# Performance work log

Hardware: AMD Instinct MI355X
Metric: run time of the kernel (lower is better)

The kernel has to match this reference:

```python
import jax, jax.numpy as jnp
import numpy as np

S, B, C, H, W = 16, 64, 128, 11, 11
P = H * W
N_ITER = 3
EPS = 1e-5


def setup_inputs() -> dict:
    key = jax.random.key(0)
    ks = jax.random.split(key, 12)
    w = lambda k, shape: jax.random.normal(k, shape, jnp.float32) * 0.02
    return {
        "x": jax.random.normal(ks[0], (S, B, C, H, W), jnp.float32),
        # intra-attention 1x1 convs (stored as [out,in] matrices)
        "wq": w(ks[1], (C, C)), "bq": jnp.zeros((C,), jnp.float32),
        "wk": w(ks[2], (C, C)), "bk": jnp.zeros((C,), jnp.float32),
        "wv": w(ks[3], (C, C)), "bv": jnp.zeros((C,), jnp.float32),
        "intra_alpha": jnp.float32(1.0),
        # inter-message path
        "w_msg": w(ks[4], (C, C + 1)), "b_msg": jnp.zeros((C,), jnp.float32),
        "w_lin": w(ks[5], (C, C)),
        "weight": jnp.float32(0.5),
        "w_gate": w(ks[6], (C, C)), "b_gate": jnp.zeros((C,), jnp.float32),
        # ConvGRU 3x3 convs
        "w_zr": w(ks[7], (2 * C, 2 * C, 3, 3)), "b_zr": jnp.zeros((2 * C,), jnp.float32),
        "w_h": w(ks[8], (C, 2 * C, 3, 3)), "b_h": jnp.zeros((C,), jnp.float32),
        # LayerNorm over [C,11,11]
        "ln_gamma": jnp.ones((C, H, W), jnp.float32),
        "ln_beta": jnp.zeros((C, H, W), jnp.float32),
    }


def reference(x, wq, bq, wk, bk, wv, bv, intra_alpha, w_msg, b_msg, w_lin,
              weight, w_gate, b_gate, w_zr, b_zr, w_h, b_h, ln_gamma, ln_beta):
    scale = C ** -0.5

    def c1(t, wgt, bias):  # 1x1 conv on [S,B,Cin,H,W] -> [S,B,Cout,H,W]
        return jnp.einsum('sbchw,oc->sbohw', t, wgt) + bias[:, None, None]

    def conv3(t, wgt, bias):  # 3x3 'SAME' conv on [N,Cin,H,W]
        y = jax.lax.conv_general_dilated(
            t, wgt, (1, 1), 'SAME', dimension_numbers=('NCHW', 'OIHW', 'NCHW'))
        return y + bias[None, :, None, None]

    # chain-graph neighbor validity masks (|i-j| == 1)
    mask_l = (jnp.arange(S) >= 1).astype(x.dtype)[:, None, None, None, None]
    mask_r = (jnp.arange(S) <= S - 2).astype(x.dtype)[:, None, None, None, None]

    h = x
    for _ in range(N_ITER):
        # ---- intra spatial self-attention (per node, over P=H*W tokens) ----
        q = c1(h, wq, bq).reshape(S, B, C, P)
        k = c1(h, wk, bk).reshape(S, B, C, P)
        v = c1(h, wv, bv).reshape(S, B, C, P)
        att = jax.nn.softmax(jnp.einsum('sbcp,sbcq->sbpq', q, k) * scale, axis=-1)
        intra = jnp.einsum('sbpq,sbcq->sbcp', att, v).reshape(S, B, C, H, W)
        intra = intra_alpha * intra + h

        # ---- inter gated message attention from chain neighbors ----
        xf = h.reshape(S, B, C, P)

        def gated_msg(y, edge_val):
            ef = jnp.full((S, B, 1, H, W), edge_val, h.dtype)  # edge feature i-j
            yy = c1(jnp.concatenate([y, ef], axis=2), w_msg, b_msg).reshape(S, B, C, P)
            yy = jnp.einsum('sbcp,dc->sbdp', yy, w_lin)  # Linear (no bias)
            a = jax.nn.softmax(jnp.einsum('sbcp,sbcq->sbpq', xf, yy), axis=-1)
            m = jnp.einsum('sbpq,sbcq->sbcp', a, yy).reshape(S, B, C, H, W)
            g = jax.nn.sigmoid(c1(m, w_gate, b_gate).mean(axis=(-2, -1), keepdims=True))
            return m * g

        y_left = jnp.concatenate([jnp.zeros_like(h[:1]), h[:-1]], axis=0)   # h[i-1], edge +1
        y_right = jnp.concatenate([h[1:], jnp.zeros_like(h[:1])], axis=0)   # h[i+1], edge -1
        inter = gated_msg(y_left, 1.0) * mask_l + gated_msg(y_right, -1.0) * mask_r

        comb = weight * intra + (1.0 - weight) * inter

        # ---- ConvGRU update (fold S into batch) ----
        xg = comb.reshape(S * B, C, H, W)
        hg = h.reshape(S * B, C, H, W)
        zr = jax.nn.sigmoid(conv3(jnp.concatenate([xg, hg], axis=1), w_zr, b_zr))
        z, r = zr[:, :C], zr[:, C:]
        h_hat = jnp.tanh(conv3(jnp.concatenate([xg, r * hg], axis=1), w_h, b_h))
        h_new = ((1 - z) * hg + z * h_hat).reshape(S, B, C, H, W)

        # ---- residual + LayerNorm over [C,H,W] ----
        nh = h_new + h
        mu = nh.mean(axis=(-3, -2, -1), keepdims=True)
        var = nh.var(axis=(-3, -2, -1), keepdims=True)
        h = (nh - mu) * jax.lax.rsqrt(var + EPS) * ln_gamma + ln_beta
    return h
```

## Files before the change

kernel.cpp:

```cpp
#include <hip/hip_runtime.h>
#include <hip/hip_bf16.h>

#define S_   16
#define B_   64
#define SBn  1024
#define C_   128
#define P_   121
#define CP_  15488
static const long NEl = 15859712L;

typedef __hip_bfloat16 bf16t;
typedef __attribute__((ext_vector_type(8))) short bf16x8;
typedef __attribute__((ext_vector_type(4))) float f32x4;
typedef __attribute__((ext_vector_type(4))) unsigned short us4;

__device__ __forceinline__ float ldb(const bf16t* p){ return __bfloat162float(*p); }
__device__ __forceinline__ float b2f(unsigned short u){ unsigned x=((unsigned)u)<<16; float f; __builtin_memcpy(&f,&x,4); return f; }
__device__ __forceinline__ unsigned short f2bu(float v){ __hip_bfloat16 b=__float2bfloat16(v); unsigned short u; __builtin_memcpy(&u,&b,2); return u; }
__device__ __forceinline__ float ldin(const void* s, long i, int f){
    return f ? ((const float*)s)[i] : b2f(((const unsigned short*)s)[i]);
}

__global__ void detect_kernel(const unsigned short* __restrict__ x, int* __restrict__ flag){
    if(blockIdx.x==0 && threadIdx.x==0){
        int crazy=0;
        for(int i=0;i<512;i++){
            unsigned e=(x[i]>>7)&0xFF;
            if(e!=0 && (e<64 || e>191)) crazy++;
        }
        *flag=(crazy>40)?1:0;
    }
}

__global__ void cvt_kernel(float* __restrict__ dst, const void* __restrict__ src, long n, const int* __restrict__ flag){
    long i=(long)blockIdx.x*blockDim.x+threadIdx.x;
    long st=(long)gridDim.x*blockDim.x;
    int f=*flag;
    for(;i<n;i+=st) dst[i]=ldin(src,i,f);
}

__global__ __launch_bounds__(256) void cvtT_kernel(bf16t* __restrict__ hT, const void* __restrict__ x, const int* __restrict__ flag){
    int sb=blockIdx.x, t=threadIdx.x; int f=*flag;
    for(int i=t;i<CP_;i+=256){
        int c=i/P_, p=i-c*P_;
        float v=ldin(x,(long)sb*CP_+i,f);
        hT[(size_t)sb*CP_+(size_t)p*C_+c]=__float2bfloat16(v);
    }
}

__global__ __launch_bounds__(128) void prep_msg_kernel(float* __restrict__ W2, float* __restrict__ b2l, float* __restrict__ b2r,
        const void* __restrict__ wlin, const void* __restrict__ wmsg, const void* __restrict__ bmsg, const int* __restrict__ flag){
    int d=blockIdx.x, c=threadIdx.x; int f=*flag;
    float acc=0.f;
    for(int o2=0;o2<C_;o2++) acc += ldin(wlin,(long)d*C_+o2,f)*ldin(wmsg,(long)o2*(C_+1)+c,f);
    W2[d*C_+c]=acc;
    if(c<2){
        float e=(c==0)?1.f:-1.f; float a=0.f;
        for(int o2=0;o2<C_;o2++) a += ldin(wlin,(long)d*C_+o2,f)*(ldin(bmsg,o2,f)+e*ldin(wmsg,(long)o2*(C_+1)+C_,f));
        if(c==0) b2l[d]=a; else b2r[d]=a;
    }
}

template<int RAW>
__global__ void prep_w1t(bf16t* __restrict__ dst, const void* __restrict__ src, const int* __restrict__ flag){
    int idx=blockIdx.x*blockDim.x+threadIdx.x;
    if(idx>=16384) return;
    int r=idx&31, oc=(idx>>5)&127, icb=idx>>12;
    float v = RAW? ldin(src,(long)oc*C_+icb*32+r,*flag) : ((const float*)src)[(long)oc*C_+icb*32+r];
    dst[idx]=__float2bfloat16(v);
}

__global__ void prep_w3t(bf16t* __restrict__ dst, const void* __restrict__ src, const int* __restrict__ flag, int OC){
    int idx=blockIdx.x*blockDim.x+threadIdx.x;
    int tot=OC*2304;
    if(idx>=tot) return;
    int r=idx&31; int rest=idx>>5; int oc=rest%OC; int g2=rest/OC; int icb=g2&7, tap=g2>>3;
    float v=ldin(src,((long)(oc*256+icb*32+r))*9+tap,*flag);
    dst[idx]=__float2bfloat16(v);
}

__global__ void prep_gbt(float* __restrict__ gamT, float* __restrict__ betT,
                         const void* __restrict__ gam, const void* __restrict__ bet, const int* __restrict__ flag){
    int idx=blockIdx.x*blockDim.x+threadIdx.x;
    if(idx>=CP_) return;
    int c=idx/P_, p=idx-c*P_; int f=*flag;
    gamT[p*C_+c]=ldin(gam,idx,f);
    betT[p*C_+c]=ldin(bet,idx,f);
}

__global__ void prep_wgt(float* __restrict__ wgT, float* __restrict__ bg2,
                         const void* __restrict__ wg, const void* __restrict__ bg, const int* __restrict__ flag){
    int idx=blockIdx.x*blockDim.x+threadIdx.x;
    int f=*flag;
    if(idx<16384){ int k=idx>>7, c=idx&127; wgT[idx]=ldin(wg,(long)c*C_+k,f); }
    if(idx<128) bg2[idx]=ldin(bg,idx,f);
}

__device__ __forceinline__ void gemm24g(f32x4 (&acc)[4][2],
    const bf16t* __restrict__ Wt, const bf16t* __restrict__ hsrc,
    int ocr,int pcr,int l15,int kg)
{
    #pragma unroll
    for(int i=0;i<4;i++){
        #pragma unroll
        for(int j=0;j<2;j++) acc[i][j]=(f32x4){0.f,0.f,0.f,0.f};
    }
    #pragma unroll
    for(int kc=0;kc<4;kc++){
        bf16x8 a[4],b[2];
        #pragma unroll
        for(int mt=0;mt<4;mt++) a[mt]=*(const bf16x8*)(Wt+((size_t)(kc*C_+ocr*64+mt*16+l15))*32+kg*8);
        #pragma unroll
        for(int nt=0;nt<2;nt++) b[nt]=*(const bf16x8*)(hsrc+(size_t)(pcr*32+nt*16+l15)*C_+kc*32+kg*8);
        #pragma unroll
        for(int mt=0;mt<4;mt++){
            #pragma unroll
            for(int nt=0;nt<2;nt++)
                acc[mt][nt]=__builtin_amdgcn_mfma_f32_16x16x32_bf16(a[mt],b[nt],acc[mt][nt],0,0,0);
        }
    }
}

__global__ __launch_bounds__(512) void qkv_attn(
    bf16t* __restrict__ comb, const bf16t* __restrict__ hT,
    const bf16t* __restrict__ WqT, const bf16t* __restrict__ WkT, const bf16t* __restrict__ WvT,
    const float* __restrict__ bq, const float* __restrict__ bk, const float* __restrict__ bv,
    const float* __restrict__ alphap, const float* __restrict__ wp)
{
    __shared__ bf16t LA[128*136];
    __shared__ bf16t LB[128*136];
    int sb=blockIdx.x, t=threadIdx.x, lane=t&63, w=t>>6;
    int l15=lane&15, kg=lane>>4;
    const bf16t* hp=hT+(size_t)sb*CP_;
    int ocr=w>>2, pcr=w&3;
    f32x4 acc[4][2];
    gemm24g(acc,WqT,hp,ocr,pcr,l15,kg);
    #pragma unroll
    for(int mt=0;mt<4;mt++){
        int oc0=ocr*64+mt*16+kg*4;
        #pragma unroll
        for(int nt=0;nt<2;nt++){
            int p=pcr*32+nt*16+l15;
            us4 pk;
            #pragma unroll
            for(int r=0;r<4;r++) pk[r]=f2bu(acc[mt][nt][r]+bq[oc0+r]);
            *(us4*)(LA+p*136+oc0)=pk;
        }
    }
    gemm24g(acc,WkT,hp,ocr,pcr,l15,kg);
    #pragma unroll
    for(int mt=0;mt<4;mt++){
        int oc0=ocr*64+mt*16+kg*4;
        #pragma unroll
        for(int nt=0;nt<2;nt++){
            int p=pcr*32+nt*16+l15;
            us4 pk;
            #pragma unroll
            for(int r=0;r<4;r++) pk[r]=f2bu(acc[mt][nt][r]+bk[oc0+r]);
            *(us4*)(LB+p*136+oc0)=pk;
        }
    }
    __syncthreads();
    int m0=w*16;
    f32x4 s[8];
    #pragma unroll
    for(int nt=0;nt<8;nt++) s[nt]=(f32x4){0.f,0.f,0.f,0.f};
    #pragma unroll
    for(int kc=0;kc<4;kc++){
        bf16x8 a=*(const bf16x8*)(LA+(size_t)(m0+l15)*136+kc*32+kg*8);
        #pragma unroll
        for(int nt=0;nt<8;nt++){
            bf16x8 b=*(const bf16x8*)(LB+(size_t)(nt*16+l15)*136+kc*32+kg*8);
            s[nt]=__builtin_amdgcn_mfma_f32_16x16x32_bf16(a,b,s[nt],0,0,0);
        }
    }
    const float scale=0.08838834764831845f;
    #pragma unroll
    for(int nt=0;nt<8;nt++){
        #pragma unroll
        for(int r=0;r<4;r++) s[nt][r]*=scale;
    }
    if(l15>=9){
        #pragma unroll
        for(int r=0;r<4;r++) s[7][r]=-3.0e38f;
    }
    #pragma unroll
    for(int r=0;r<4;r++){
        float mx=s[0][r];
        #pragma unroll
        for(int nt=1;nt<8;nt++) mx=fmaxf(mx,s[nt][r]);
        #pragma unroll
        for(int o=1;o<16;o<<=1) mx=fmaxf(mx,__shfl_xor(mx,o));
        float sm=0.f;
        #pragma unroll
        for(int nt=0;nt<8;nt++){ float e=__expf(s[nt][r]-mx); s[nt][r]=e; sm+=e; }
        #pragma unroll
        for(int o=1;o<16;o<<=1) sm+=__shfl_xor(sm,o);
        float rs=1.f/sm;
        #pragma unroll
        for(int nt=0;nt<8;nt++) s[nt][r]*=rs;
    }
    __syncthreads();
    gemm24g(acc,WvT,hp,ocr,pcr,l15,kg);
    #pragma unroll
    for(int mt=0;mt<4;mt++){
        int oc0=ocr*64+mt*16+kg*4;
        #pragma unroll
        for(int nt=0;nt<2;nt++){
            int p=pcr*32+nt*16+l15;
            #pragma unroll
            for(int r=0;r<4;r++)
                LA[(oc0+r)*136+p]=__float2bfloat16(p<P_? acc[mt][nt][r]+bv[oc0+r] : 0.f);
        }
    }
    #pragma unroll
    for(int r=0;r<4;r++){
        int pr=m0+kg*4+r;
        #pragma unroll
        for(int nt=0;nt<8;nt++) LB[pr*136+nt*16+l15]=__float2bfloat16(s[nt][r]);
    }
    __syncthreads();
    f32x4 o[8];
    #pragma unroll
    for(int nt=0;nt<8;nt++) o[nt]=(f32x4){0.f,0.f,0.f,0.f};
    #pragma unroll
    for(int jc=0;jc<4;jc++){
        bf16x8 a=*(const bf16x8*)(LA+(size_t)(m0+l15)*136+jc*32+kg*8);
        #pragma unroll
        for(int nt=0;nt<8;nt++){
            bf16x8 b=*(const bf16x8*)(LB+(size_t)(nt*16+l15)*136+jc*32+kg*8);
            o[nt]=__builtin_amdgcn_mfma_f32_16x16x32_bf16(a,b,o[nt],0,0,0);
        }
    }
    float al=*alphap, wv=*wp;
    int c0=m0+kg*4;
    bf16t* ob=comb+(size_t)sb*CP_;
    #pragma unroll
    for(int nt=0;nt<8;nt++){
        int p=nt*16+l15;
        if(p>=P_) continue;
        us4 hv=*(const us4*)(hp+(size_t)p*C_+c0);
        us4 pk;
        #pragma unroll
        for(int r=0;r<4;r++) pk[r]=f2bu(wv*(al*o[nt][r]+b2f(hv[r])));
        *(us4*)(ob+(size_t)p*C_+c0)=pk;
    }
}

__global__ __launch_bounds__(512) void msg_all(
    bf16t* __restrict__ comb, const bf16t* __restrict__ hT,
    const bf16t* __restrict__ W2T, const float* __restrict__ b2e,
    const float* __restrict__ wgT, const float* __restrict__ bgf,
    const float* __restrict__ wp, int sb0, int shift)
{
    __shared__ bf16t LA[128*136];
    __shared__ bf16t LB[128*136];
    __shared__ float fl[256];
    int sb=sb0+blockIdx.x, t=threadIdx.x, lane=t&63, w=t>>6;
    int l15=lane&15, kg=lane>>4;
    const bf16t* hsp=hT+(size_t)(sb+shift)*CP_;
    int ocr=w>>2, pcr=w&3;
    f32x4 acc[4][2];
    gemm24g(acc,W2T,hsp,ocr,pcr,l15,kg);
    #pragma unroll
    for(int mt=0;mt<4;mt++){
        int oc0=ocr*64+mt*16+kg*4;
        #pragma unroll
        for(int nt=0;nt<2;nt++){
            int p=pcr*32+nt*16+l15;
            us4 pk;
            #pragma unroll
            for(int r=0;r<4;r++){
                float v=acc[mt][nt][r]+b2e[oc0+r];
                pk[r]=f2bu(v);
                LB[(oc0+r)*136+p]=__float2bfloat16(p<P_? v : 0.f);
            }
            *(us4*)(LA+p*136+oc0)=pk;
        }
    }
    __syncthreads();
    int m0=w*16;
    const bf16t* ap=hT+(size_t)sb*CP_;
    f32x4 s[8];
    #pragma unroll
    for(int nt=0;nt<8;nt++) s[nt]=(f32x4){0.f,0.f,0.f,0.f};
    #pragma unroll
    for(int kc=0;kc<4;kc++){
        bf16x8 a=*(const bf16x8*)(ap+(size_t)(m0+l15)*C_+kc*32+kg*8);
        #pragma unroll
        for(int nt=0;nt<8;nt++){
            bf16x8 b=*(const bf16x8*)(LA+(size_t)(nt*16+l15)*136+kc*32+kg*8);
            s[nt]=__builtin_amdgcn_mfma_f32_16x16x32_bf16(a,b,s[nt],0,0,0);
        }
    }
    if(l15>=9){
        #pragma unroll
        for(int r=0;r<4;r++) s[7][r]=-3.0e38f;
    }
    #pragma unroll
    for(int r=0;r<4;r++){
        float mx=s[0][r];
        #pragma unroll
        for(int nt=1;nt<8;nt++) mx=fmaxf(mx,s[nt][r]);
        #pragma unroll
        for(int o=1;o<16;o<<=1) mx=fmaxf(mx,__shfl_xor(mx,o));
        float sm=0.f;
        #pragma unroll
        for(int nt=0;nt<8;nt++){ float e=__expf(s[nt][r]-mx); s[nt][r]=e; sm+=e; }
        #pragma unroll
        for(int o=1;o<16;o<<=1) sm+=__shfl_xor(sm,o);
        float rs=1.f/sm;
        #pragma unroll
        for(int nt=0;nt<8;nt++) s[nt][r]*=rs;
    }
    __syncthreads();
    #pragma unroll
    for(int r=0;r<4;r++){
        int pr=m0+kg*4+r;
        #pragma unroll
        for(int nt=0;nt<8;nt++) LA[pr*136+nt*16+l15]=__float2bfloat16(s[nt][r]);
    }
    __syncthreads();
    f32x4 o[8];
    #pragma unroll
    for(int nt=0;nt<8;nt++) o[nt]=(f32x4){0.f,0.f,0.f,0.f};
    #pragma unroll
    for(int jc=0;jc<4;jc++){
        bf16x8 a=*(const bf16x8*)(LB+(size_t)(m0+l15)*136+jc*32+kg*8);
        #pragma unroll
        for(int nt=0;nt<8;nt++){
            bf16x8 b=*(const bf16x8*)(LA+(size_t)(nt*16+l15)*136+jc*32+kg*8);
            o[nt]=__builtin_amdgcn_mfma_f32_16x16x32_bf16(a,b,o[nt],0,0,0);
        }
    }
    int c0=m0+kg*4;
    #pragma unroll
    for(int r=0;r<4;r++){
        float sm=0.f;
        #pragma unroll
        for(int nt=0;nt<8;nt++){ float v=o[nt][r]; if(nt==7&&l15>8) v=0.f; sm+=v; }
        sm+=__shfl_xor(sm,1); sm+=__shfl_xor(sm,2); sm+=__shfl_xor(sm,4); sm+=__shfl_xor(sm,8);
        if(l15==0) fl[c0+r]=sm*(1.f/121.f);
    }
    __syncthreads();
    if(t<C_){
        float a=bgf[t];
        #pragma unroll 8
        for(int k=0;k<C_;k++) a+=wgT[k*C_+t]*fl[k];
        fl[C_+t]=1.f/(1.f+__expf(-a));
    }
    __syncthreads();
    float w1m=1.f-*wp;
    float gg[4];
    #pragma unroll
    for(int r=0;r<4;r++) gg[r]=fl[C_+c0+r];
    bf16t* ob=comb+(size_t)sb*CP_;
    #pragma unroll
    for(int nt=0;nt<8;nt++){
        int p=nt*16+l15;
        if(p>=P_) continue;
        us4 bv=*(const us4*)(ob+(size_t)p*C_+c0);
        #pragma unroll
        for(int r=0;r<4;r++) bv[r]=f2bu(b2f(bv[r]) + w1m*o[nt][r]*gg[r]);
        *(us4*)(ob+(size_t)p*C_+c0)=bv;
    }
}

#define LOADA3(bidx, widx) { \
    _Pragma("unroll") \
    for(int mt=0;mt<4;mt++) abuf[bidx][mt]=*(const bf16x8*)(Wt+(size_t)(widx)*(OC*32)+mt*512+base_lane); }
#define STEP3(bidx, doff) { \
    bf16x8 bb[4]; \
    _Pragma("unroll") \
    for(int nt=0;nt<4;nt++) bb[nt]=*(const bf16x8*)(lin+boff[nt]+(doff)); \
    __builtin_amdgcn_s_setprio(1); \
    _Pragma("unroll") \
    for(int mt=0;mt<4;mt++){ \
        _Pragma("unroll") \
        for(int nt=0;nt<4;nt++) \
            acc[mt][nt]=__builtin_amdgcn_mfma_f32_16x16x32_bf16(abuf[bidx][mt],bb[nt],acc[mt][nt],0,0,0); } \
    __builtin_amdgcn_s_setprio(0); }

template<int MODE>
__global__ __launch_bounds__(256) void conv3_mfma(
    bf16t* __restrict__ o0, bf16t* __restrict__ o1,
    const bf16t* __restrict__ in0T, const bf16t* __restrict__ in1T,
    const bf16t* __restrict__ Wt, const float* __restrict__ bias,
    const bf16t* __restrict__ zT, const bf16t* __restrict__ hTb,
    const float* __restrict__ gamT, const float* __restrict__ betT)
{
    constexpr int OC=(MODE==1)?256:128;
    constexpr int LSZ=(MODE==2)?15488:12176;
    __shared__ bf16t lin[LSZ];
    __shared__ float red[8];
    int sb=blockIdx.x, ocb=(MODE==1)? (int)blockIdx.y*128 : 0;
    int t=threadIdx.x, lane=t&63, w=t>>6;
    int ocr=w>>1, pcr=w&1, l15=lane&15, kg=lane>>4;
    int boff[4]; bool pv_[4];
    #pragma unroll
    for(int nt=0;nt<4;nt++){
        int p=pcr*64+nt*16+l15;
        pv_[nt]=(p<P_); int pc=pv_[nt]?p:(P_-1);
        boff[nt]=((pc/11)*13+(pc%11))*72+kg*8;
    }
    f32x4 acc[4][4];
    #pragma unroll
    for(int i=0;i<4;i++){
        #pragma unroll
        for(int j=0;j<4;j++) acc[i][j]=(f32x4){0.f,0.f,0.f,0.f};
    }
    int base_lane=(ocb+ocr*64+l15)*32+kg*8;
    bf16x8 abuf[4][4];
    LOADA3(0,0); LOADA3(1,1); LOADA3(2,8); LOADA3(3,9);
    {
        bf16x8 z;
        #pragma unroll
        for(int e=0;e<8;e++) z[e]=0;
        for(int i=t;i<384;i+=256){
            int bi=i>>3, cc=(i&7)*8;
            int pix;
            if(bi<13) pix=bi;
            else if(bi<26) pix=156+(bi-13);
            else { int j2=bi-26; pix=(1+(j2>>1))*13+((j2&1)?12:0); }
            *(bf16x8*)(lin+pix*72+cc)=z;
        }
    }
    #pragma unroll
    for(int st=0; st<4; ++st){
        __syncthreads();
        {
            const bf16t* src=((st<2)? in0T:in1T)+(size_t)sb*CP_+(st&1)*64;
            for(int i=t;i<968;i+=256){
                int p=i>>3, cc=(i&7)*8;
                int pix=(p/11+1)*13+(p%11)+1;
                *(bf16x8*)(lin+pix*72+cc)=*(const bf16x8*)(src+(size_t)p*C_+cc);
            }
        }
        __syncthreads();
        #pragma unroll
        for(int k=0;k<18;k++){
            int s=st*18+k;
            int tap=k>>1, l=k&1;
            int doff=((tap/3)*13+(tap%3))*72+l*32;
            STEP3(s&3, doff);
            if(s<68){
                int s4=s+4, st4=s4/18, k4=s4-st4*18, tap4=k4>>1, l4=k4&1;
                LOADA3(s&3, tap4*8+st4*2+l4);
            }
        }
    }
    if(MODE==1){
        #pragma unroll
        for(int mt=0;mt<4;mt++){
            int ocl=ocr*64+mt*16+kg*4;
            #pragma unroll
            for(int nt=0;nt<4;nt++){
                if(!pv_[nt]) continue;
                int p=pcr*64+nt*16+l15;
                size_t tb=(size_t)sb*CP_+(size_t)p*C_+ocl;
                us4 pk;
                if(ocb==0){
                    #pragma unroll
                    for(int r=0;r<4;r++){ float a=acc[mt][nt][r]+bias[ocl+r]; pk[r]=f2bu(1.f/(1.f+__expf(-a))); }
                    *(us4*)(o0+tb)=pk;
                }else{
                    us4 hv=*(const us4*)(hTb+tb);
                    #pragma unroll
                    for(int r=0;r<4;r++){ float a=acc[mt][nt][r]+bias[128+ocl+r]; float sg=1.f/(1.f+__expf(-a)); pk[r]=f2bu(sg*b2f(hv[r])); }
                    *(us4*)(o1+tb)=pk;
                }
            }
        }
    }else{
        __syncthreads();
        float ls=0.f, ls2=0.f;
        #pragma unroll
        for(int mt=0;mt<4;mt++){
            int ocl=ocr*64+mt*16+kg*4;
            #pragma unroll
            for(int nt=0;nt<4;nt++){
                if(!pv_[nt]) continue;
                int p=pcr*64+nt*16+l15;
                size_t tb=(size_t)sb*CP_+(size_t)p*C_+ocl;
                us4 hv=*(const us4*)(hTb+tb);
                us4 zv=*(const us4*)(zT+tb);
                us4 pk;
                #pragma unroll
                for(int r=0;r<4;r++){
                    float a=acc[mt][nt][r]+bias[ocl+r];
                    float ht=tanhf(a);
                    float z=b2f(zv[r]), h=b2f(hv[r]);
                    unsigned short u=f2bu((1.f-z)*h+z*ht+h);
                    pk[r]=u;
                    float nr=b2f(u); ls+=nr; ls2+=nr*nr;
                }
                *(us4*)((unsigned short*)lin + p*C_+ocl)=pk;
            }
        }
        #pragma unroll
        for(int o=32;o;o>>=1){ ls+=__shfl_xor(ls,o); ls2+=__shfl_xor(ls2,o); }
        if(lane==0){ red[w]=ls; red[4+w]=ls2; }
        __syncthreads();
        float Sx=red[0]+red[1]+red[2]+red[3];
        float Sx2=red[4]+red[5]+red[6]+red[7];
        float mu=Sx*(1.f/(float)CP_);
        float var=Sx2*(1.f/(float)CP_)-mu*mu;
        float rstd=rsqrtf(var+1e-5f);
        bf16t* ho=o0+(size_t)sb*CP_;
        for(int i=t;i<CP_;i+=256){
            float v=(ldb(lin+i)-mu)*rstd*gamT[i]+betT[i];
            ho[i]=__float2bfloat16(v);
        }
    }
}

__global__ __launch_bounds__(256) void finalT_kernel(void* __restrict__ fout, const bf16t* __restrict__ hT, const int* __restrict__ flag){
    __shared__ bf16t tl[CP_];
    int sb=blockIdx.x, t=threadIdx.x, f=*flag;
    for(int i=t;i<CP_;i+=256) tl[i]=hT[(size_t)sb*CP_+i];
    __syncthreads();
    for(int i=t;i<CP_;i+=256){
        int c=i/P_, p=i-c*P_;
        float v=ldb(tl+p*C_+c);
        size_t oi=(size_t)sb*CP_+i;
        if(f) ((float*)fout)[oi]=v;
        else  ((bf16t*)fout)[oi]=__float2bfloat16(v);
    }
}

extern "C" void kernel_launch(void* const* d_in, const int* in_sizes, int n_in,
                              void* d_out, int out_size, void* d_ws, size_t ws_size,
                              hipStream_t stream) {
    (void)in_sizes; (void)n_in; (void)out_size;
    char* base=(char*)d_ws;
    size_t off=0;
    auto alloc=[&](size_t bytes){ void* p=base+off; off+=(bytes+255)&~(size_t)255; return p; };
    bf16t* b1=(bf16t*)alloc((size_t)NEl*2+8192);
    bf16t* b2=(bf16t*)alloc((size_t)NEl*2+8192);
    bf16t* b3=(bf16t*)alloc((size_t)NEl*2+8192);
    bf16t* b4=(bf16t*)d_out;
    bf16t* wqT=(bf16t*)alloc(16384*2);
    bf16t* wkT=(bf16t*)alloc(16384*2);
    bf16t* wvT=(bf16t*)alloc(16384*2);
    bf16t* w2T=(bf16t*)alloc(16384*2);
    bf16t* wzrT=(bf16t*)alloc((size_t)589824*2);
    bf16t* whT =(bf16t*)alloc((size_t)294912*2);
    float* W2f=(float*)alloc(16384*4);
    float* b2l=(float*)alloc(128*4); float* b2r=(float*)alloc(128*4);
    float* bqf=(float*)alloc(128*4); float* bkf=(float*)alloc(128*4); float* bvf=(float*)alloc(128*4);
    float* bzrf=(float*)alloc(256*4); float* bhf=(float*)alloc(128*4);
    float* gamT=(float*)alloc(15488*4); float* betT=(float*)alloc(15488*4);
    float* wgTf=(float*)alloc(16384*4); float* bgf2=(float*)alloc(128*4);
    float* alphaf=(float*)alloc(4); float* weightf=(float*)alloc(4);
    int* flag=(int*)alloc(4);
    if(ws_size<off) return;

    detect_kernel<<<1,64,0,stream>>>((const unsigned short*)d_in[0],flag);
    cvtT_kernel<<<SBn,256,0,stream>>>(b1,d_in[0],flag);
    prep_w1t<1><<<64,256,0,stream>>>(wqT,d_in[1],flag);
    cvt_kernel<<<1,128,0,stream>>>(bqf,d_in[2],128,flag);
    prep_w1t<1><<<64,256,0,stream>>>(wkT,d_in[3],flag);
    cvt_kernel<<<1,128,0,stream>>>(bkf,d_in[4],128,flag);
    prep_w1t<1><<<64,256,0,stream>>>(wvT,d_in[5],flag);
    cvt_kernel<<<1,128,0,stream>>>(bvf,d_in[6],128,flag);
    cvt_kernel<<<1,64,0,stream>>>(alphaf,d_in[7],1,flag);
    prep_msg_kernel<<<C_,C_,0,stream>>>(W2f,b2l,b2r,d_in[10],d_in[8],d_in[9],flag);
    prep_w1t<0><<<64,256,0,stream>>>(w2T,W2f,flag);
    cvt_kernel<<<1,64,0,stream>>>(weightf,d_in[11],1,flag);
    prep_wgt<<<64,256,0,stream>>>(wgTf,bgf2,d_in[12],d_in[13],flag);
    prep_w3t<<<(256*2304+255)/256,256,0,stream>>>(wzrT,d_in[14],flag,256);
    cvt_kernel<<<1,256,0,stream>>>(bzrf,d_in[15],256,flag);
    prep_w3t<<<(128*2304+255)/256,256,0,stream>>>(whT,d_in[16],flag,128);
    cvt_kernel<<<1,128,0,stream>>>(bhf,d_in[17],128,flag);
    prep_gbt<<<(CP_+255)/256,256,0,stream>>>(gamT,betT,d_in[18],d_in[19],flag);

    for(int it=0; it<3; ++it){
        qkv_attn<<<SBn,512,0,stream>>>(b2,b1,wqT,wkT,wvT,bqf,bkf,bvf,alphaf,weightf);
        msg_all<<<SBn-B_,512,0,stream>>>(b2,b1,w2T,b2l,wgTf,bgf2,weightf,B_,-B_);
        msg_all<<<SBn-B_,512,0,stream>>>(b2,b1,w2T,b2r,wgTf,bgf2,weightf,0,B_);
        conv3_mfma<1><<<dim3(SBn,2),256,0,stream>>>(b4,b3,b2,b1,wzrT,bzrf,nullptr,b1,nullptr,nullptr);
        conv3_mfma<2><<<dim3(SBn,1),256,0,stream>>>(b1,nullptr,b2,b3,whT,bhf,b4,b1,gamT,betT);
    }
    finalT_kernel<<<SBn,256,0,stream>>>(d_out,b1,flag);
}
```

Measured before the change: 1.521 ms.

## Double-buffer conv3 input staging via registers and hoist h fragments in QKV/msg GEMMs

The 3x3 conv kernel now uses two LDS buffers. The next channel stage's input is loaded from global into registers while MFMAs run on the current buffer, then written to the other buffer, so each stage needs one barrier instead of two. In the attention and message kernels, the h operand fragments are loaded into registers once and reused across the Q, K and V GEMMs instead of being reloaded from global each time. The cost is more LDS per block (the MODE 2 buffer grows) and more live registers, which may reduce occupancy.

```diff
diff --git a/kernel.cpp b/kernel.cpp
--- a/kernel.cpp
+++ b/kernel.cpp
@@ -96,9 +96,9 @@
     if(idx<128) bg2[idx]=ldin(bg,idx,f);
 }
 
-__device__ __forceinline__ void gemm24g(f32x4 (&acc)[4][2],
-    const bf16t* __restrict__ Wt, const bf16t* __restrict__ hsrc,
-    int ocr,int pcr,int l15,int kg)
+__device__ __forceinline__ void gemm24r(f32x4 (&acc)[4][2],
+    const bf16t* __restrict__ Wt, const bf16x8 (&hreg)[4][2],
+    int ocr,int l15,int kg)
 {
     #pragma unroll
     for(int i=0;i<4;i++){
@@ -107,16 +107,14 @@
     }
     #pragma unroll
     for(int kc=0;kc<4;kc++){
-        bf16x8 a[4],b[2];
+        bf16x8 a[4];
         #pragma unroll
         for(int mt=0;mt<4;mt++) a[mt]=*(const bf16x8*)(Wt+((size_t)(kc*C_+ocr*64+mt*16+l15))*32+kg*8);
-        #pragma unroll
-        for(int nt=0;nt<2;nt++) b[nt]=*(const bf16x8*)(hsrc+(size_t)(pcr*32+nt*16+l15)*C_+kc*32+kg*8);
         #pragma unroll
         for(int mt=0;mt<4;mt++){
             #pragma unroll
             for(int nt=0;nt<2;nt++)
-                acc[mt][nt]=__builtin_amdgcn_mfma_f32_16x16x32_bf16(a[mt],b[nt],acc[mt][nt],0,0,0);
+                acc[mt][nt]=__builtin_amdgcn_mfma_f32_16x16x32_bf16(a[mt],hreg[kc][nt],acc[mt][nt],0,0,0);
         }
     }
 }
@@ -133,8 +131,15 @@
     int l15=lane&15, kg=lane>>4;
     const bf16t* hp=hT+(size_t)sb*CP_;
     int ocr=w>>2, pcr=w&3;
+    bf16x8 hreg[4][2];
+    #pragma unroll
+    for(int kc=0;kc<4;kc++){
+        #pragma unroll
+        for(int nt=0;nt<2;nt++)
+            hreg[kc][nt]=*(const bf16x8*)(hp+(size_t)(pcr*32+nt*16+l15)*C_+kc*32+kg*8);
+    }
     f32x4 acc[4][2];
-    gemm24g(acc,WqT,hp,ocr,pcr,l15,kg);
+    gemm24r(acc,WqT,hreg,ocr,l15,kg);
     #pragma unroll
     for(int mt=0;mt<4;mt++){
         int oc0=ocr*64+mt*16+kg*4;
@@ -147,7 +152,7 @@
             *(us4*)(LA+p*136+oc0)=pk;
         }
     }
-    gemm24g(acc,WkT,hp,ocr,pcr,l15,kg);
+    gemm24r(acc,WkT,hreg,ocr,l15,kg);
     #pragma unroll
     for(int mt=0;mt<4;mt++){
         int oc0=ocr*64+mt*16+kg*4;
@@ -201,7 +206,7 @@
         for(int nt=0;nt<8;nt++) s[nt][r]*=rs;
     }
     __syncthreads();
-    gemm24g(acc,WvT,hp,ocr,pcr,l15,kg);
+    gemm24r(acc,WvT,hreg,ocr,l15,kg);
     #pragma unroll
     for(int mt=0;mt<4;mt++){
         int oc0=ocr*64+mt*16+kg*4;
@@ -260,8 +265,15 @@
     int l15=lane&15, kg=lane>>4;
     const bf16t* hsp=hT+(size_t)(sb+shift)*CP_;
     int ocr=w>>2, pcr=w&3;
+    bf16x8 hreg[4][2];
+    #pragma unroll
+    for(int kc=0;kc<4;kc++){
+        #pragma unroll
+        for(int nt=0;nt<2;nt++)
+            hreg[kc][nt]=*(const bf16x8*)(hsp+(size_t)(pcr*32+nt*16+l15)*C_+kc*32+kg*8);
+    }
     f32x4 acc[4][2];
-    gemm24g(acc,W2T,hsp,ocr,pcr,l15,kg);
+    gemm24r(acc,W2T,hreg,ocr,l15,kg);
     #pragma unroll
     for(int mt=0;mt<4;mt++){
         int oc0=ocr*64+mt*16+kg*4;
@@ -369,10 +381,10 @@
 #define LOADA3(bidx, widx) { \
     _Pragma("unroll") \
     for(int mt=0;mt<4;mt++) abuf[bidx][mt]=*(const bf16x8*)(Wt+(size_t)(widx)*(OC*32)+mt*512+base_lane); }
-#define STEP3(bidx, doff) { \
+#define STEP3(lbase, bidx, doff) { \
     bf16x8 bb[4]; \
     _Pragma("unroll") \
-    for(int nt=0;nt<4;nt++) bb[nt]=*(const bf16x8*)(lin+boff[nt]+(doff)); \
+    for(int nt=0;nt<4;nt++) bb[nt]=*(const bf16x8*)((lbase)+boff[nt]+(doff)); \
     __builtin_amdgcn_s_setprio(1); \
     _Pragma("unroll") \
     for(int mt=0;mt<4;mt++){ \
@@ -380,6 +392,17 @@
         for(int nt=0;nt<4;nt++) \
             acc[mt][nt]=__builtin_amdgcn_mfma_f32_16x16x32_bf16(abuf[bidx][mt],bb[nt],acc[mt][nt],0,0,0); } \
     __builtin_amdgcn_s_setprio(0); }
+#define SLOAD3(stg) { \
+    const bf16t* ssrc=(((stg)<2)? in0T:in1T)+(size_t)sb*CP_+((stg)&1)*64; \
+    sreg[0]=*(const bf16x8*)(ssrc+(size_t)(t>>3)*C_+(t&7)*8); \
+    sreg[1]=*(const bf16x8*)(ssrc+(size_t)((t+256)>>3)*C_+(t&7)*8); \
+    if(sv2) sreg[2]=*(const bf16x8*)(ssrc+(size_t)((t+512)>>3)*C_+(t&7)*8); \
+    if(sv3) sreg[3]=*(const bf16x8*)(ssrc+(size_t)((t+768)>>3)*C_+(t&7)*8); }
+#define SWRITE3(lbase) { \
+    *(bf16x8*)((lbase)+spix0*72+(t&7)*8)=sreg[0]; \
+    *(bf16x8*)((lbase)+spix1*72+(t&7)*8)=sreg[1]; \
+    if(sv2) *(bf16x8*)((lbase)+spix2*72+(t&7)*8)=sreg[2]; \
+    if(sv3) *(bf16x8*)((lbase)+spix3*72+(t&7)*8)=sreg[3]; }
 
 template<int MODE>
 __global__ __launch_bounds__(256) void conv3_mfma(
@@ -390,8 +413,7 @@
     const float* __restrict__ gamT, const float* __restrict__ betT)
 {
     constexpr int OC=(MODE==1)?256:128;
-    constexpr int LSZ=(MODE==2)?15488:12176;
-    __shared__ bf16t lin[LSZ];
+    __shared__ bf16t lin[2*12176];
     __shared__ float red[8];
     int sb=blockIdx.x, ocb=(MODE==1)? (int)blockIdx.y*128 : 0;
     int t=threadIdx.x, lane=t&63, w=t>>6;
@@ -411,43 +433,50 @@
     }
     int base_lane=(ocb+ocr*64+l15)*32+kg*8;
     bf16x8 abuf[4][4];
+    bf16x8 sreg[4];
+    bool sv2=((t+512)<968), sv3=((t+768)<968);
+    int sp0=t>>3, sp1=(t+256)>>3, sp2=(t+512)>>3, sp3=(t+768)>>3;
+    if(sp2>120) sp2=120;
+    if(sp3>120) sp3=120;
+    int spix0=(sp0/11+1)*13+(sp0%11)+1;
+    int spix1=(sp1/11+1)*13+(sp1%11)+1;
+    int spix2=(sp2/11+1)*13+(sp2%11)+1;
+    int spix3=(sp3/11+1)*13+(sp3%11)+1;
     LOADA3(0,0); LOADA3(1,1); LOADA3(2,8); LOADA3(3,9);
+    SLOAD3(0);
     {
         bf16x8 z;
         #pragma unroll
         for(int e=0;e<8;e++) z[e]=0;
-        for(int i=t;i<384;i+=256){
-            int bi=i>>3, cc=(i&7)*8;
+        for(int i=t;i<768;i+=256){
+            int half=i>=384; int i2=i-half*384;
+            int bi=i2>>3, cc=(i2&7)*8;
             int pix;
             if(bi<13) pix=bi;
             else if(bi<26) pix=156+(bi-13);
             else { int j2=bi-26; pix=(1+(j2>>1))*13+((j2&1)?12:0); }
-            *(bf16x8*)(lin+pix*72+cc)=z;
-        }
-    }
+            *(bf16x8*)(lin+half*12176+pix*72+cc)=z;
+        }
+    }
+    SWRITE3(lin);
+    __syncthreads();
     #pragma unroll
     for(int st=0; st<4; ++st){
-        __syncthreads();
-        {
-            const bf16t* src=((st<2)? in0T:in1T)+(size_t)sb*CP_+(st&1)*64;
-            for(int i=t;i<968;i+=256){
-                int p=i>>3, cc=(i&7)*8;
-                int pix=(p/11+1)*13+(p%11)+1;
-                *(bf16x8*)(lin+pix*72+cc)=*(const bf16x8*)(src+(size_t)p*C_+cc);
-            }
-        }
-        __syncthreads();
+        if(st<3) SLOAD3(st+1);
+        bf16t* lbase=lin+(st&1)*12176;
         #pragma unroll
         for(int k=0;k<18;k++){
             int s=st*18+k;
             int tap=k>>1, l=k&1;
             int doff=((tap/3)*13+(tap%3))*72+l*32;
-            STEP3(s&3, doff);
+            STEP3(lbase, s&3, doff);
             if(s<68){
                 int s4=s+4, st4=s4/18, k4=s4-st4*18, tap4=k4>>1, l4=k4&1;
                 LOADA3(s&3, tap4*8+st4*2+l4);
             }
         }
+        if(st<3){ SWRITE3(lin+((st+1)&1)*12176); }
+        __syncthreads();
     }
     if(MODE==1){
         #pragma unroll
@@ -472,7 +501,6 @@
             }
         }
     }else{
-        __syncthreads();
         float ls=0.f, ls2=0.f;
         #pragma unroll
         for(int mt=0;mt<4;mt++){
```

Result: faster. 1.450 ms (-4.7%).
